# Optimization experiments

Measured on AMD Instinct MI355X. Metric: run time of the kernel, lower is better.

The kernel has to match this reference:

```python
import jax, jax.numpy as jnp
import numpy as np

N = 4096          # number of video frames (n)
M = 1024          # input feature size (m)
D = 1024          # output_size; must equal M for the grid_sample offset math
APPERTURE = 256   # band half-width: logits with |i-j| >= APPERTURE are masked
SCALE = 0.06      # Q scaling from the original module


def _grid_sample_bilinear(img, gx, gy):
    """F.grid_sample(img[None,None], grid, mode='bilinear', align_corners=True).
    img: (H, W); gx, gy: (H, W) normalized coords in [-1, 1].
    gx indexes the W (last) axis, gy the H axis, matching torch's grid layout."""
    H, W = img.shape
    ix = (gx + 1.0) * (W - 1) * 0.5
    iy = (gy + 1.0) * (H - 1) * 0.5
    ix0 = jnp.floor(ix)
    iy0 = jnp.floor(iy)
    wx = ix - ix0  # weight for the +1 neighbor along W
    wy = iy - iy0  # weight for the +1 neighbor along H
    ix0i = jnp.clip(ix0.astype(jnp.int32), 0, W - 1)
    ix1i = jnp.clip(ix0i + 1, 0, W - 1)
    iy0i = jnp.clip(iy0.astype(jnp.int32), 0, H - 1)
    iy1i = jnp.clip(iy0i + 1, 0, H - 1)
    v00 = img[iy0i, ix0i]
    v01 = img[iy0i, ix1i]
    v10 = img[iy1i, ix0i]
    v11 = img[iy1i, ix1i]
    return (1.0 - wy) * ((1.0 - wx) * v00 + wx * v01) + wy * ((1.0 - wx) * v10 + wx * v11)


def setup_inputs() -> dict:
    key = jax.random.key(0)
    ks = jax.random.split(key, 8)
    s = 0.02
    f32 = jnp.float32
    return {
        "x": jax.random.normal(ks[0], (N, M), f32),
        "Wq": s * jax.random.normal(ks[1], (M, D), f32),
        "Wk": s * jax.random.normal(ks[2], (M, D), f32),
        "Wv": s * jax.random.normal(ks[3], (M, D), f32),
        "Wofx": s * jax.random.normal(ks[4], (D, D), f32),
        "bofx": jnp.zeros((D,), f32),
        "Wofy": s * jax.random.normal(ks[5], (D, D), f32),
        "bofy": jnp.zeros((D,), f32),
        "Wout": s * jax.random.normal(ks[6], (D, M), f32),
    }


def reference(x, Wq, Wk, Wv, Wofx, bofx, Wofy, bofy, Wout):
    H, W = x.shape  # H = n frames, W = m features
    Q = x @ Wq                       # (n, D)
    # offsets are computed from the UNscaled Q (scaling happens later in torch)
    ofx = Q @ Wofx + bofx            # (n, D) == (H, W) since D == W
    ofy = Q @ Wofy + bofy
    # base grid: channel 0 = 2*i/H - 1 (row), channel 1 = 2*j/W - 1 (col);
    # grid_sample reads channel 0 as the x (W-axis) coordinate, channel 1 as y.
    rows = jnp.arange(H, dtype=x.dtype)[:, None]
    cols = jnp.arange(W, dtype=x.dtype)[None, :]
    gx = jnp.clip(2.0 * rows / H - 1.0 + ofx, -1.0, 1.0)  # (H, W)
    gy = jnp.clip(2.0 * cols / W - 1.0 + ofy, -1.0, 1.0)  # (H, W)
    x_new = _grid_sample_bilinear(x, gx, gy)              # (H, W)
    K = x_new @ Wk                   # (n, D)
    V = x_new @ Wv                   # (n, D)
    logits = (SCALE * Q) @ K.T       # (n, n)
    idx = jnp.arange(H)
    band_mask = jnp.abs(idx[:, None] - idx[None, :]) >= APPERTURE
    logits = jnp.where(band_mask, -jnp.inf, logits)
    att = jax.nn.softmax(logits, axis=-1)  # (n, n); dropout is identity at eval
    # torch: y = (V.T @ att).T  ==  att.T @ V  (note the transpose of att!)
    y = att.T @ V                    # (n, D)
    y = y @ Wout                     # (n, m)
    return y, att
```

## Files before the change

### kernel.cpp

```cpp
#include <hip/hip_runtime.h>
#include <hip/hip_bf16.h>
#include <math.h>

#define NN 4096
#define MM 1024
#define BANDP 512

typedef float f4v __attribute__((ext_vector_type(4)));
typedef float f32x4 __attribute__((ext_vector_type(4)));
typedef short bf16x8 __attribute__((ext_vector_type(8)));
typedef short s4v __attribute__((ext_vector_type(4)));

__device__ __forceinline__ short f2b(float f) {
    union { float f; unsigned u; } v; v.f = f;
    unsigned r = v.u + 0x7fffu + ((v.u >> 16) & 1u);
    return (short)(r >> 16);
}
__device__ __forceinline__ float b2f(short s) {
    union { unsigned u; float f; } v;
    v.u = ((unsigned)(unsigned short)s) << 16;
    return v.f;
}

__device__ __forceinline__ void gl2lds16(const void* g, void* l) {
    __builtin_amdgcn_global_load_lds(
        (const __attribute__((address_space(1))) void*)g,
        (__attribute__((address_space(3))) void*)l, 16, 0, 0);
}

__global__ __launch_bounds__(256)
void split_x_k(const float* __restrict__ s, short* __restrict__ h,
               short* __restrict__ l)
{
    const int i = (blockIdx.x * 256 + threadIdx.x) << 2;
    f4v v = *(const f4v*)&s[i];
    s4v hv, lv;
    #pragma unroll
    for (int q = 0; q < 4; ++q) {
        hv[q] = f2b(v[q]);
        lv[q] = f2b(v[q] - b2f(hv[q]));
    }
    *(s4v*)&h[i] = hv;
    *(s4v*)&l[i] = lv;
}

__global__ __launch_bounds__(256)
void trsplit_k(const float* __restrict__ W, short* __restrict__ Th,
               short* __restrict__ Tl)
{
    __shared__ float tile[32][33];
    const int bx = blockIdx.x << 5, by = blockIdx.y << 5;
    const int tx = threadIdx.x, ty = threadIdx.y;
    #pragma unroll
    for (int r = ty; r < 32; r += 8)
        tile[r][tx] = W[(size_t)(by + r) * MM + bx + tx];
    __syncthreads();
    #pragma unroll
    for (int r = ty; r < 32; r += 8) {
        const float v = tile[tx][r];
        const short h = f2b(v);
        Th[(size_t)(bx + r) * MM + by + tx] = h;
        Tl[(size_t)(bx + r) * MM + by + tx] = f2b(v - b2f(h));
    }
}

__global__ __launch_bounds__(256)
void transpose_f32_bf16(const float* __restrict__ W, short* __restrict__ Wt)
{
    __shared__ float tile[32][33];
    const int bx = blockIdx.x << 5, by = blockIdx.y << 5;
    const int tx = threadIdx.x, ty = threadIdx.y;
    #pragma unroll
    for (int r = ty; r < 32; r += 8)
        tile[r][tx] = W[(size_t)(by + r) * MM + bx + tx];
    __syncthreads();
    #pragma unroll
    for (int r = ty; r < 32; r += 8)
        Wt[(size_t)(bx + r) * MM + by + tx] = f2b(tile[tx][r]);
}

template<bool BIAS>
__global__ __launch_bounds__(256, 2)
void gemm_split(const short* __restrict__ Ah, const short* __restrict__ Al,
                const short* __restrict__ Bth, const short* __restrict__ Btl,
                const float* __restrict__ bias0, const float* __restrict__ bias1,
                short* __restrict__ outH, short* __restrict__ outL, int N)
{
    __shared__ short As[2][2][128 * 32];
    __shared__ short Bs[2][2][128 * 32];

    const int t  = threadIdx.x;
    const int l  = t & 63;
    const int w  = t >> 6;
    const int wm = w >> 1, wn = w & 1;
    const int lr = l & 15;
    const int lk = (l >> 4) << 3;

    const int i0 = blockIdx.y << 7;
    const int bn = blockIdx.x << 7;

    const int sr = t >> 2;
    const int sk = (t & 3) << 3;

    const short* aH = Ah  + (size_t)(i0 + sr) * MM + sk;
    const short* aL = Al  + (size_t)(i0 + sr) * MM + sk;
    const short* bH = Bth + (size_t)(bn + sr) * MM + sk;
    const short* bL = Btl + (size_t)(bn + sr) * MM + sk;

    f32x4 acc[4][4] = {};

    auto stage = [&](int sb, int k0) {
        gl2lds16(aH + k0,           &As[sb][0][t * 8]);
        gl2lds16(aH + 64 * MM + k0, &As[sb][0][2048 + t * 8]);
        gl2lds16(aL + k0,           &As[sb][1][t * 8]);
        gl2lds16(aL + 64 * MM + k0, &As[sb][1][2048 + t * 8]);
        gl2lds16(bH + k0,           &Bs[sb][0][t * 8]);
        gl2lds16(bH + 64 * MM + k0, &Bs[sb][0][2048 + t * 8]);
        gl2lds16(bL + k0,           &Bs[sb][1][t * 8]);
        gl2lds16(bL + 64 * MM + k0, &Bs[sb][1][2048 + t * 8]);
    };
    stage(0, 0);
    __syncthreads();

    for (int kt = 0; kt < 32; ++kt) {
        const int cur = kt & 1;
        if (kt + 1 < 32) stage(cur ^ 1, (kt + 1) << 5);
        bf16x8 ah[4], al[4], bh[4], bl[4];
        #pragma unroll
        for (int i = 0; i < 4; ++i) {
            ah[i] = *(const bf16x8*)&As[cur][0][(wm * 64 + i * 16 + lr) * 32 + lk];
            al[i] = *(const bf16x8*)&As[cur][1][(wm * 64 + i * 16 + lr) * 32 + lk];
        }
        #pragma unroll
        for (int j = 0; j < 4; ++j) {
            bh[j] = *(const bf16x8*)&Bs[cur][0][(wn * 64 + j * 16 + lr) * 32 + lk];
            bl[j] = *(const bf16x8*)&Bs[cur][1][(wn * 64 + j * 16 + lr) * 32 + lk];
        }
        #pragma unroll
        for (int i = 0; i < 4; ++i)
            #pragma unroll
            for (int j = 0; j < 4; ++j) {
                acc[i][j] = __builtin_amdgcn_mfma_f32_16x16x32_bf16(ah[i], bl[j], acc[i][j], 0, 0, 0);
                acc[i][j] = __builtin_amdgcn_mfma_f32_16x16x32_bf16(al[i], bh[j], acc[i][j], 0, 0, 0);
                acc[i][j] = __builtin_amdgcn_mfma_f32_16x16x32_bf16(ah[i], bh[j], acc[i][j], 0, 0, 0);
            }
        __syncthreads();
    }

    const int rb = (l >> 4) << 2;
    #pragma unroll
    for (int i = 0; i < 4; ++i)
        #pragma unroll
        for (int j = 0; j < 4; ++j) {
            const int n = bn + wn * 64 + j * 16 + lr;
            float bv = 0.f;
            if (BIAS) bv = (n < 1024) ? bias0[n] : bias1[n - 1024];
            #pragma unroll
            for (int r = 0; r < 4; ++r) {
                const int m = i0 + wm * 64 + i * 16 + rb + r;
                const float v = acc[i][j][r] + bv;
                const short h = f2b(v);
                outH[(size_t)m * N + n] = h;
                outL[(size_t)m * N + n] = f2b(v - b2f(h));
            }
        }
}

__global__ __launch_bounds__(256)
void grid_sample_k(const short* __restrict__ xh, const short* __restrict__ ofh,
                   const short* __restrict__ ofl, short* __restrict__ xnb)
{
    const int i = blockIdx.x;
    const int tid = threadIdx.x;
    const int j4 = tid << 2;

    const short* rh = ofh + (size_t)i * 2048;
    const short* rl = ofl + (size_t)i * 2048;
    s4v hx = *(const s4v*)&rh[j4];
    s4v lx = *(const s4v*)&rl[j4];
    s4v hy = *(const s4v*)&rh[1024 + j4];
    s4v ly = *(const s4v*)&rl[1024 + j4];
    s4v out;

    const float gxb = (2.0f * (float)i) / (float)NN - 1.0f;

    #pragma unroll
    for (int q = 0; q < 4; ++q) {
        const int j = j4 + q;
        float gx = gxb + b2f(hx[q]) + b2f(lx[q]);
        gx = fminf(fmaxf(gx, -1.0f), 1.0f);
        float gy = (2.0f * (float)j) / (float)MM - 1.0f + b2f(hy[q]) + b2f(ly[q]);
        gy = fminf(fmaxf(gy, -1.0f), 1.0f);

        const float ixf = (gx + 1.0f) * 511.5f;
        const float iyf = (gy + 1.0f) * 2047.5f;
        const float ix0 = floorf(ixf);
        const float iy0 = floorf(iyf);
        const float wx = ixf - ix0;
        const float wy = iyf - iy0;
        int ix0i = (int)ix0; ix0i = max(0, min(ix0i, MM - 1));
        int iy0i = (int)iy0; iy0i = max(0, min(iy0i, NN - 1));
        const int ix1i = min(ix0i + 1, MM - 1);
        const int iy1i = min(iy0i + 1, NN - 1);

        const short* r0 = xh + (size_t)iy0i * MM;
        const short* r1 = xh + (size_t)iy1i * MM;
        const float v00 = b2f(r0[ix0i]), v01 = b2f(r0[ix1i]);
        const float v10 = b2f(r1[ix0i]), v11 = b2f(r1[ix1i]);
        out[q] = f2b((1.0f - wy) * ((1.0f - wx) * v00 + wx * v01)
                   + wy * ((1.0f - wx) * v10 + wx * v11));
    }
    *(s4v*)&xnb[(size_t)i * MM + j4] = out;
}

template<int MODE>
__global__ __launch_bounds__(256, 2)
void mfma_gemm(const short* __restrict__ A, const short* __restrict__ Bt,
               void* __restrict__ C0, void* __restrict__ C1)
{
    __shared__ short As[2][128 * 32];
    __shared__ short Bs[2][128 * 32];

    const int t  = threadIdx.x;
    const int l  = t & 63;
    const int w  = t >> 6;
    const int wm = w >> 1, wn = w & 1;
    const int lr = l & 15;
    const int lk = (l >> 4) << 3;

    const int i0 = blockIdx.y << 7;
    const int bn = blockIdx.x << 7;
    const int jb = (MODE == 3) ? (i0 - 256 + bn) : bn;

    const int sr = t >> 2;
    const int sk = (t & 3) << 3;

    const short* aS = A + (size_t)(i0 + sr) * MM + sk;
    int br0 = jb + sr, br1 = jb + sr + 64;
    if (MODE == 3) {
        br0 = min(max(br0, 0), NN - 1);
        br1 = min(max(br1, 0), NN - 1);
    }
    const short* bS0 = Bt + (size_t)br0 * MM + sk;
    const short* bS1 = Bt + (size_t)br1 * MM + sk;

    f32x4 acc[4][4] = {};

    auto stage = [&](int sb, int k0) {
        gl2lds16(aS + k0,           &As[sb][0] + t * 8);
        gl2lds16(aS + 64 * MM + k0, &As[sb][0] + 2048 + t * 8);
        gl2lds16(bS0 + k0,          &Bs[sb][0] + t * 8);
        gl2lds16(bS1 + k0,          &Bs[sb][0] + 2048 + t * 8);
    };
    stage(0, 0);
    __syncthreads();

    for (int kt = 0; kt < 32; ++kt) {
        const int cur = kt & 1;
        if (kt + 1 < 32) stage(cur ^ 1, (kt + 1) << 5);
        bf16x8 a[4], b[4];
        #pragma unroll
        for (int i = 0; i < 4; ++i)
            a[i] = *(const bf16x8*)&As[cur][(wm * 64 + i * 16 + lr) * 32 + lk];
        #pragma unroll
        for (int j = 0; j < 4; ++j)
            b[j] = *(const bf16x8*)&Bs[cur][(wn * 64 + j * 16 + lr) * 32 + lk];
        #pragma unroll
        for (int i = 0; i < 4; ++i)
            #pragma unroll
            for (int j = 0; j < 4; ++j)
                acc[i][j] = __builtin_amdgcn_mfma_f32_16x16x32_bf16(a[i], b[j], acc[i][j], 0, 0, 0);
        __syncthreads();
    }

    const int rb = (l >> 4) << 2;
    #pragma unroll
    for (int i = 0; i < 4; ++i) {
        #pragma unroll
        for (int j = 0; j < 4; ++j) {
            const int nl = wn * 64 + j * 16 + lr;
            if (MODE == 4 && bn + nl >= 1024) {
                const int m0 = i0 + wm * 64 + i * 16 + rb;
                s4v o;
                #pragma unroll
                for (int r = 0; r < 4; ++r) o[r] = f2b(acc[i][j][r]);
                *(s4v*)&((short*)C1)[(size_t)(bn + nl - 1024) * NN + m0] = o;
            } else {
                #pragma unroll
                for (int r = 0; r < 4; ++r) {
                    const int m = i0 + wm * 64 + i * 16 + rb + r;
                    const float v = acc[i][j][r];
                    if (MODE == 4) {
                        ((short*)C0)[(size_t)m * MM + bn + nl] = f2b(v);
                    } else if (MODE == 2) {
                        ((float*)C0)[(size_t)m * MM + bn + nl] = v;
                    } else if (MODE == 3) {
                        const int jj = jb + nl;
                        const int ci = jj - m + 255;
                        if (ci >= 0 && ci <= 510)
                            ((float*)C0)[(size_t)m * BANDP + ci] =
                                (jj >= 0 && jj < NN) ? 0.06f * v : -INFINITY;
                    }
                }
            }
        }
    }
}

__global__ __launch_bounds__(256)
void band_softmax(const float* __restrict__ band, float* __restrict__ att,
                  short* __restrict__ bandT)
{
    const int i = blockIdx.x;
    const int tid = threadIdx.x;
    const float* brow = band + (size_t)i * BANDP;

    float v0 = brow[tid];
    float v1 = (tid < 255) ? brow[tid + 256] : -INFINITY;

    float m = fmaxf(v0, v1);
    #pragma unroll
    for (int o = 32; o >= 1; o >>= 1) m = fmaxf(m, __shfl_xor(m, o));
    __shared__ float redm[4], reds[4];
    const int wv = tid >> 6, ln = tid & 63;
    if (ln == 0) redm[wv] = m;
    __syncthreads();
    m = fmaxf(fmaxf(redm[0], redm[1]), fmaxf(redm[2], redm[3]));

    float p0 = expf(v0 - m);
    float p1 = (tid < 255) ? expf(v1 - m) : 0.f;
    float s = p0 + p1;
    #pragma unroll
    for (int o = 32; o >= 1; o >>= 1) s += __shfl_xor(s, o);
    if (ln == 0) reds[wv] = s;
    __syncthreads();
    s = reds[0] + reds[1] + reds[2] + reds[3];
    const float rinv = 1.0f / s;
    p0 *= rinv; p1 *= rinv;

    float* arow = att + (size_t)i * NN;
    f4v z = {0.f, 0.f, 0.f, 0.f};
    #pragma unroll
    for (int q = 0; q < 4; ++q)
        *(f4v*)&arow[(q * 256 + tid) << 2] = z;
    __syncthreads();
    int j = i + tid - 255;
    if (j >= 0 && j < NN) {
        arow[j] = p0;
        bandT[(size_t)j * 768 + (i - (j & ~7) + 384)] = f2b(p0);
    }
    j = i + tid + 1;
    if (tid < 255 && j >= 0 && j < NN) {
        arow[j] = p1;
        bandT[(size_t)j * 768 + (i - (j & ~7) + 384)] = f2b(p1);
    }
}

__global__ __launch_bounds__(256, 2)
void attT_v_mfma(const short* __restrict__ bandT, const short* __restrict__ Vt,
                 short* __restrict__ y1b)
{
    const int t = threadIdx.x, l = t & 63, w = t >> 6;
    const int wm = w >> 1, wn = w & 1;
    const int lr = l & 15, lk = (l >> 4) << 3;
    const int r0 = blockIdx.y << 7;
    const int n0 = blockIdx.x << 6;

    f32x4 acc[4][2] = {};
    for (int ks = 0; ks < 20; ++ks) {
        const int j0 = r0 - 256 + (ks << 5);
        if (j0 < 0 || j0 >= NN) continue;
        bf16x8 b[2];
        #pragma unroll
        for (int j = 0; j < 2; ++j)
            b[j] = *(const bf16x8*)&Vt[(size_t)(n0 + wn * 32 + j * 16 + lr) * NN + j0 + lk];
        #pragma unroll
        for (int i = 0; i < 4; ++i) {
            const int r = r0 + wm * 64 + i * 16 + lr;
            const int cc = j0 + lk - (r & ~7) + 384;
            bf16x8 a = *(const bf16x8*)&bandT[(size_t)r * 768 + cc];
            #pragma unroll
            for (int j = 0; j < 2; ++j)
                acc[i][j] = __builtin_amdgcn_mfma_f32_16x16x32_bf16(a, b[j], acc[i][j], 0, 0, 0);
        }
    }
    const int rb = (l >> 4) << 2;
    #pragma unroll
    for (int i = 0; i < 4; ++i)
        #pragma unroll
        for (int j = 0; j < 2; ++j)
            #pragma unroll
            for (int r = 0; r < 4; ++r)
                y1b[(size_t)(r0 + wm * 64 + i * 16 + rb + r) * MM + n0 + wn * 32 + j * 16 + lr]
                    = f2b(acc[i][j][r]);
}

extern "C" void kernel_launch(void* const* d_in, const int* in_sizes, int n_in,
                              void* d_out, int out_size, void* d_ws, size_t ws_size,
                              hipStream_t stream)
{
    const float* x    = (const float*)d_in[0];
    const float* Wq   = (const float*)d_in[1];
    const float* Wk   = (const float*)d_in[2];
    const float* Wv   = (const float*)d_in[3];
    const float* Wofx = (const float*)d_in[4];
    const float* bofx = (const float*)d_in[5];
    const float* Wofy = (const float*)d_in[6];
    const float* bofy = (const float*)d_in[7];
    const float* Wout = (const float*)d_in[8];

    float* y_out   = (float*)d_out;
    float* att_out = (float*)d_out + (size_t)NN * MM;

    char* wsb = (char*)d_ws;
    const size_t MB = 1024 * 1024;
    short* xh      = (short*)(wsb + 0);
    short* Qh      = (short*)(wsb + 8 * MB);
    short* Ql      = (short*)(wsb + 16 * MB);
    short* xl      = (short*)(wsb + 24 * MB);
    short* WqTh    = (short*)(wsb + 32 * MB);
    short* WqTl    = (short*)(wsb + 34 * MB);
    short* WofxyTh = (short*)(wsb + 24 * MB);
    short* WofxyTl = (short*)(wsb + 28 * MB);
    short* ofxyh   = (short*)(wsb + 32 * MB);
    short* ofxyl   = (short*)(wsb + 48 * MB);
    short* xnb     = (short*)(wsb + 16 * MB);
    short* WkvT    = (short*)(wsb + 0);
    short* WoutT   = (short*)(wsb + 4 * MB);
    short* Kb      = (short*)(wsb + 24 * MB);
    short* Vtb     = (short*)(wsb + 32 * MB);
    float* band    = (float*)(wsb + 40 * MB);
    short* bandT   = (short*)(wsb + 48 * MB);
    short* y1b     = (short*)(wsb + 16 * MB);

    const dim3 blk(256);
    const dim3 tgrid(32, 32), tblk(32, 8);

    split_x_k<<<dim3(4096), blk, 0, stream>>>(x, xh, xl);
    trsplit_k<<<tgrid, tblk, 0, stream>>>(Wq, WqTh, WqTl);
    gemm_split<false><<<dim3(8, 32), blk, 0, stream>>>(
        xh, xl, WqTh, WqTl, nullptr, nullptr, Qh, Ql, 1024);
    trsplit_k<<<tgrid, tblk, 0, stream>>>(Wofx, WofxyTh, WofxyTl);
    trsplit_k<<<tgrid, tblk, 0, stream>>>(Wofy, WofxyTh + 1024 * 1024, WofxyTl + 1024 * 1024);
    gemm_split<true><<<dim3(16, 32), blk, 0, stream>>>(
        Qh, Ql, WofxyTh, WofxyTl, bofx, bofy, ofxyh, ofxyl, 2048);

    grid_sample_k<<<dim3(NN), blk, 0, stream>>>(xh, ofxyh, ofxyl, xnb);

    transpose_f32_bf16<<<tgrid, tblk, 0, stream>>>(Wk, WkvT);
    transpose_f32_bf16<<<tgrid, tblk, 0, stream>>>(Wv, WkvT + 1024 * 1024);
    transpose_f32_bf16<<<tgrid, tblk, 0, stream>>>(Wout, WoutT);

    mfma_gemm<4><<<dim3(16, 32), blk, 0, stream>>>(xnb, WkvT, Kb, Vtb);
    mfma_gemm<3><<<dim3(5, 32), blk, 0, stream>>>(Qh, Kb, band, nullptr);
    hipMemsetAsync(bandT, 0, (size_t)NN * 768 * sizeof(short), stream);
    band_softmax<<<dim3(NN), blk, 0, stream>>>(band, att_out, bandT);
    attT_v_mfma<<<dim3(16, 32), blk, 0, stream>>>(bandT, Vtb, y1b);
    mfma_gemm<2><<<dim3(8, 32), blk, 0, stream>>>(y1b, WoutT, y_out, nullptr);
}
```

Before: 334.5 us.

## Swizzle LDS tiles and overlap next-tile loads with partial vmcnt waits

Both GEMM kernels get an XOR swizzle on the 16-byte k-chunk, applied on the global source offset and on the LDS read index, to cut LDS bank conflicts on the fragment reads. The full __syncthreads is replaced by explicit s_waitcnt vmcnt(N) plus s_barrier, so each iteration waits only for the current tile's async global-to-LDS loads while the next tile's loads stay in flight. The MFMA section is also wrapped in s_setprio to favour the math waves. The hand-coded vmcnt counts are a risk: they assume the compiler emits no other outstanding vector memory ops, otherwise the wait is wrong and data can race.

```diff
diff --git a/kernel.cpp b/kernel.cpp
--- a/kernel.cpp
+++ b/kernel.cpp
@@ -27,6 +27,10 @@
         (const __attribute__((address_space(1))) void*)g,
         (__attribute__((address_space(3))) void*)l, 16, 0, 0);
 }
+
+#define WAIT_VM8() asm volatile("s_waitcnt vmcnt(8)" ::: "memory")
+#define WAIT_VM4() asm volatile("s_waitcnt vmcnt(4)" ::: "memory")
+#define WAIT_VM0() asm volatile("s_waitcnt vmcnt(0)" ::: "memory")
 
 __global__ __launch_bounds__(256)
 void split_x_k(const float* __restrict__ s, short* __restrict__ h,
@@ -95,12 +99,13 @@
     const int wm = w >> 1, wn = w & 1;
     const int lr = l & 15;
     const int lk = (l >> 4) << 3;
+    const int lks = lk ^ (((l >> 1) & 3) << 3);
 
     const int i0 = blockIdx.y << 7;
     const int bn = blockIdx.x << 7;
 
     const int sr = t >> 2;
-    const int sk = (t & 3) << 3;
+    const int sk = (((t & 3) ^ ((t >> 3) & 3)) << 3);
 
     const short* aH = Ah  + (size_t)(i0 + sr) * MM + sk;
     const short* aL = Al  + (size_t)(i0 + sr) * MM + sk;
@@ -120,22 +125,26 @@
         gl2lds16(bL + 64 * MM + k0, &Bs[sb][1][2048 + t * 8]);
     };
     stage(0, 0);
-    __syncthreads();
 
     for (int kt = 0; kt < 32; ++kt) {
         const int cur = kt & 1;
-        if (kt + 1 < 32) stage(cur ^ 1, (kt + 1) << 5);
+        if (kt + 1 < 32) { stage(cur ^ 1, (kt + 1) << 5); WAIT_VM8(); }
+        else             { WAIT_VM0(); }
+        __builtin_amdgcn_s_barrier();
+        __builtin_amdgcn_sched_barrier(0);
+
         bf16x8 ah[4], al[4], bh[4], bl[4];
         #pragma unroll
         for (int i = 0; i < 4; ++i) {
-            ah[i] = *(const bf16x8*)&As[cur][0][(wm * 64 + i * 16 + lr) * 32 + lk];
-            al[i] = *(const bf16x8*)&As[cur][1][(wm * 64 + i * 16 + lr) * 32 + lk];
+            ah[i] = *(const bf16x8*)&As[cur][0][(wm * 64 + i * 16 + lr) * 32 + lks];
+            al[i] = *(const bf16x8*)&As[cur][1][(wm * 64 + i * 16 + lr) * 32 + lks];
         }
         #pragma unroll
         for (int j = 0; j < 4; ++j) {
-            bh[j] = *(const bf16x8*)&Bs[cur][0][(wn * 64 + j * 16 + lr) * 32 + lk];
-            bl[j] = *(const bf16x8*)&Bs[cur][1][(wn * 64 + j * 16 + lr) * 32 + lk];
+            bh[j] = *(const bf16x8*)&Bs[cur][0][(wn * 64 + j * 16 + lr) * 32 + lks];
+            bl[j] = *(const bf16x8*)&Bs[cur][1][(wn * 64 + j * 16 + lr) * 32 + lks];
         }
+        __builtin_amdgcn_s_setprio(1);
         #pragma unroll
         for (int i = 0; i < 4; ++i)
             #pragma unroll
@@ -144,7 +153,8 @@
                 acc[i][j] = __builtin_amdgcn_mfma_f32_16x16x32_bf16(al[i], bh[j], acc[i][j], 0, 0, 0);
                 acc[i][j] = __builtin_amdgcn_mfma_f32_16x16x32_bf16(ah[i], bh[j], acc[i][j], 0, 0, 0);
             }
-        __syncthreads();
+        __builtin_amdgcn_s_setprio(0);
+        __builtin_amdgcn_s_barrier();
     }
 
     const int rb = (l >> 4) << 2;
@@ -227,13 +237,14 @@
     const int wm = w >> 1, wn = w & 1;
     const int lr = l & 15;
     const int lk = (l >> 4) << 3;
+    const int lks = lk ^ (((l >> 1) & 3) << 3);
 
     const int i0 = blockIdx.y << 7;
     const int bn = blockIdx.x << 7;
     const int jb = (MODE == 3) ? (i0 - 256 + bn) : bn;
 
     const int sr = t >> 2;
-    const int sk = (t & 3) << 3;
+    const int sk = (((t & 3) ^ ((t >> 3) & 3)) << 3);
 
     const short* aS = A + (size_t)(i0 + sr) * MM + sk;
     int br0 = jb + sr, br1 = jb + sr + 64;
@@ -253,24 +264,29 @@
         gl2lds16(bS1 + k0,          &Bs[sb][0] + 2048 + t * 8);
     };
     stage(0, 0);
-    __syncthreads();
 
     for (int kt = 0; kt < 32; ++kt) {
         const int cur = kt & 1;
-        if (kt + 1 < 32) stage(cur ^ 1, (kt + 1) << 5);
+        if (kt + 1 < 32) { stage(cur ^ 1, (kt + 1) << 5); WAIT_VM4(); }
+        else             { WAIT_VM0(); }
+        __builtin_amdgcn_s_barrier();
+        __builtin_amdgcn_sched_barrier(0);
+
         bf16x8 a[4], b[4];
         #pragma unroll
         for (int i = 0; i < 4; ++i)
-            a[i] = *(const bf16x8*)&As[cur][(wm * 64 + i * 16 + lr) * 32 + lk];
+            a[i] = *(const bf16x8*)&As[cur][(wm * 64 + i * 16 + lr) * 32 + lks];
         #pragma unroll
         for (int j = 0; j < 4; ++j)
-            b[j] = *(const bf16x8*)&Bs[cur][(wn * 64 + j * 16 + lr) * 32 + lk];
+            b[j] = *(const bf16x8*)&Bs[cur][(wn * 64 + j * 16 + lr) * 32 + lks];
+        __builtin_amdgcn_s_setprio(1);
         #pragma unroll
         for (int i = 0; i < 4; ++i)
             #pragma unroll
             for (int j = 0; j < 4; ++j)
                 acc[i][j] = __builtin_amdgcn_mfma_f32_16x16x32_bf16(a[i], b[j], acc[i][j], 0, 0, 0);
-        __syncthreads();
+        __builtin_amdgcn_s_setprio(0);
+        __builtin_amdgcn_s_barrier();
     }
 
     const int rb = (l >> 4) << 2;
```

After: 328.9 us. About the same (-1.7%).
